# Kernel tuning notes

Hardware: AMD Instinct MI355X
Metric: run time of the kernel (lower is better)

Reference implementation:

```python
import jax, jax.numpy as jnp
import numpy as np

B, K = 2048, 256
ED = RD = HD = 256
AD = ED + RD          # action_dim = 512
IN = ED + HD + RD     # 768
NUM_E, NUM_R = 100000, 500
HUGE = jnp.float32(1e31)  # ops.HUGE_INT


def setup_inputs() -> dict:
    key = jax.random.key(0)
    ks = jax.random.split(key, 12)
    s = 0.05  # keep logits in a sane range
    E = jax.random.normal(ks[0], (B, ED), jnp.float32)
    H = jax.random.normal(ks[1], (B, HD), jnp.float32)
    Q = jax.random.normal(ks[2], (B, RD), jnp.float32)
    W1 = jax.random.normal(ks[3], (AD, IN), jnp.float32) * s
    b1 = jnp.zeros((AD,), jnp.float32)
    W2 = jax.random.normal(ks[4], (AD, AD), jnp.float32) * s
    b2 = jnp.zeros((AD,), jnp.float32)
    emb_r = jax.random.normal(ks[5], (NUM_R, RD), jnp.float32) * s
    emb_e = jax.random.normal(ks[6], (NUM_E, ED), jnp.float32) * s
    # binary action mask (variable-size action spaces, padded); col 0 always valid
    action_mask = (jax.random.uniform(ks[7], (B, K)) > 0.3).astype(jnp.float32)
    action_mask = action_mask.at[:, 0].set(1.0)
    r_space = jax.random.randint(ks[8], (B, K), 0, NUM_R)
    e_space = jax.random.randint(ks[9], (B, K), 0, NUM_E)
    return {"E": E, "H": H, "Q": Q, "W1": W1, "b1": b1, "W2": W2, "b2": b2,
            "emb_r": emb_r, "emb_e": emb_e, "action_mask": action_mask,
            "r_space": r_space, "e_space": e_space}


def reference(E, H, Q, W1, b1, W2, b2, emb_r, emb_e, action_mask, r_space, e_space):
    # state MLP: X = W2Dropout(W2(relu(W1(cat([E, H, Q])))))  (dropout = identity at eval)
    X = jnp.concatenate([E, H, Q], axis=-1)           # [B, IN]
    X = jax.nn.relu(X @ W1.T + b1)                    # [B, AD]
    X2 = X @ W2.T + b2                                # [B, AD]
    # gather action embeddings: A = cat([emb_r[r], emb_e[e]])  [B, K, AD]
    A = jnp.concatenate([emb_r[r_space], emb_e[e_space]], axis=-1)
    # masked softmax over action space
    scores = jnp.einsum('bkd,bd->bk', A, X2) - (1.0 - action_mask) * HUGE
    action_dist = jax.nn.softmax(scores, axis=-1)     # [B, K]
    entropy = -jnp.sum(action_dist * jnp.log(action_dist + 1e-20), axis=-1)  # [B]
    return action_dist, entropy
```

## Files before the change

kernel.cpp:

```cpp
#include <hip/hip_runtime.h>
#include <hip/hip_bf16.h>
#include <hip/hip_fp8.h>
#include <math.h>

#define B_   2048
#define K_   256
#define AD_  512
#define IN_  768
#define NR_  500
#define NRP_ 512
#define NE_  100000

typedef __attribute__((ext_vector_type(8))) short short8;
typedef __attribute__((ext_vector_type(4))) float float4v;

__device__ __forceinline__ unsigned short f2bf(float f) {
    unsigned int u = __float_as_uint(f);
    unsigned int r = u + 0x7FFF + ((u >> 16) & 1);
    return (unsigned short)(r >> 16);
}
__device__ __forceinline__ float bf2f(short s) {
    return __uint_as_float(((unsigned int)(unsigned short)s) << 16);
}
__device__ __forceinline__ unsigned char f2fp8(float f) {
    __hip_fp8_e4m3 t(f);
    return (unsigned char)t.__x;
}
__device__ __forceinline__ float fp8tof(unsigned int byte) {
    __hip_fp8_e4m3 t; t.__x = (__hip_fp8_storage_t)byte; return (float)t;
}
__device__ __forceinline__ float dot4_fp8(unsigned int d, const float* x) {
    return fp8tof(d & 0xffu)         * x[0] + fp8tof((d >> 8) & 0xffu)  * x[1]
         + fp8tof((d >> 16) & 0xffu) * x[2] + fp8tof(d >> 24)           * x[3];
}

#define EE_N4 (NE_ * 256 / 4)
#define X_N4  (B_ * IN_ / 4)
#define W1_N4 (AD_ * IN_ / 4)
#define W2_N4 (AD_ * AD_ / 4)
#define ER_N4 (NR_ * 256 / 4)
#define PREP_TOTAL (EE_N4 + X_N4 + W1_N4 + W2_N4 + ER_N4)
__global__ __launch_bounds__(256) void prep_kernel(
    const float* __restrict__ E, const float* __restrict__ H,
    const float* __restrict__ Q, const float* __restrict__ W1,
    const float* __restrict__ W2, const float* __restrict__ emb_r,
    const float* __restrict__ emb_e,
    ushort* __restrict__ Xb, ushort* __restrict__ W1b,
    ushort* __restrict__ W2b, ushort* __restrict__ emb_rb,
    unsigned char* __restrict__ emb_e8)
{
    int t = blockIdx.x * 256 + threadIdx.x;
    if (t < EE_N4) {
        const float4 v = *(const float4*)&emb_e[(size_t)t * 4];
        uchar4 o;
        o.x = f2fp8(v.x); o.y = f2fp8(v.y); o.z = f2fp8(v.z); o.w = f2fp8(v.w);
        *(uchar4*)&emb_e8[(size_t)t * 4] = o;
        return;
    }
    t -= EE_N4;
    const float* src; ushort* dst; long off;
    if (t < X_N4) {
        const int base = t * 4;
        const int row = base / IN_, col = base % IN_;
        src = (col < 256) ? &E[row * 256 + col]
            : (col < 512) ? &H[row * 256 + col - 256]
                          : &Q[row * 256 + col - 512];
        const float4 v = *(const float4*)src;
        ushort4 o;
        o.x = f2bf(v.x); o.y = f2bf(v.y); o.z = f2bf(v.z); o.w = f2bf(v.w);
        *(ushort4*)&Xb[base] = o;
        return;
    }
    t -= X_N4;
    if (t < W1_N4)                 { src = W1;    dst = W1b;    off = t; }
    else if (t < W1_N4 + W2_N4)    { src = W2;    dst = W2b;    off = t - W1_N4; }
    else if (t < W1_N4 + W2_N4 + ER_N4) { src = emb_r; dst = emb_rb; off = t - W1_N4 - W2_N4; }
    else return;
    const float4 v = *(const float4*)&src[off * 4];
    ushort4 o;
    o.x = f2bf(v.x); o.y = f2bf(v.y); o.z = f2bf(v.z); o.w = f2bf(v.w);
    *(ushort4*)&dst[off * 4] = o;
}

template<int K, bool RELU, bool OUT_BF16, bool BIAS, bool EMIT_RHALF>
__global__ __launch_bounds__(256) void gemm_bf16_kernel(
    const ushort* __restrict__ A, const ushort* __restrict__ Bw,
    const float* __restrict__ bias, ushort* __restrict__ outb,
    float* __restrict__ outf, ushort* __restrict__ rhalf)
{
    constexpr int PITCH = 72;
    __shared__ ushort Asl[2][64 * PITCH];
    __shared__ ushort Bsl[2][64 * PITCH];
    const int tid = threadIdx.x;
    const int lane = tid & 63, w = tid >> 6;
    const int n0 = blockIdx.x * 64, m0 = blockIdx.y * 64;
    const int lrow = tid >> 2, lcg = (tid & 3) * 16;
    const int q = lane >> 4, l16 = lane & 15;

    const ushort* aptr = &A[(size_t)(m0 + lrow) * K + lcg];
    const ushort* bptr = &Bw[(size_t)(n0 + lrow) * K + lcg];

    short8 ra0 = *(const short8*)aptr;
    short8 ra1 = *(const short8*)(aptr + 8);
    short8 rb0 = *(const short8*)bptr;
    short8 rb1 = *(const short8*)(bptr + 8);
    *(short8*)&Asl[0][lrow * PITCH + lcg]     = ra0;
    *(short8*)&Asl[0][lrow * PITCH + lcg + 8] = ra1;
    *(short8*)&Bsl[0][lrow * PITCH + lcg]     = rb0;
    *(short8*)&Bsl[0][lrow * PITCH + lcg + 8] = rb1;

    float4v acc[4] = {};
    int buf = 0;
    __syncthreads();
    for (int k0 = 0; k0 < K; k0 += 64) {
        if (k0 + 64 < K) {
            ra0 = *(const short8*)(aptr + k0 + 64);
            ra1 = *(const short8*)(aptr + k0 + 64 + 8);
            rb0 = *(const short8*)(bptr + k0 + 64);
            rb1 = *(const short8*)(bptr + k0 + 64 + 8);
        }
        #pragma unroll
        for (int kh = 0; kh < 64; kh += 32) {
            const short8 af = *(const short8*)&Asl[buf][(w * 16 + l16) * PITCH + kh + q * 8];
            #pragma unroll
            for (int jn = 0; jn < 4; ++jn) {
                const short8 bfr = *(const short8*)&Bsl[buf][(jn * 16 + l16) * PITCH + kh + q * 8];
                acc[jn] = __builtin_amdgcn_mfma_f32_16x16x32_bf16(af, bfr, acc[jn], 0, 0, 0);
            }
        }
        if (k0 + 64 < K) {
            *(short8*)&Asl[buf ^ 1][lrow * PITCH + lcg]     = ra0;
            *(short8*)&Asl[buf ^ 1][lrow * PITCH + lcg + 8] = ra1;
            *(short8*)&Bsl[buf ^ 1][lrow * PITCH + lcg]     = rb0;
            *(short8*)&Bsl[buf ^ 1][lrow * PITCH + lcg + 8] = rb1;
            __syncthreads();
            buf ^= 1;
        }
    }
    #pragma unroll
    for (int jn = 0; jn < 4; ++jn) {
        const int n = n0 + jn * 16 + l16;
        const float bn = BIAS ? bias[n] : 0.0f;
        #pragma unroll
        for (int r = 0; r < 4; ++r) {
            const int m = m0 + w * 16 + q * 4 + r;
            float c = acc[jn][r] + bn;
            if (RELU) c = fmaxf(c, 0.0f);
            if (OUT_BF16) outb[(size_t)m * AD_ + n] = f2bf(c);
            else if (!EMIT_RHALF || n >= 256) outf[(size_t)m * AD_ + n] = c;
            if (EMIT_RHALF && n < 256) rhalf[(size_t)m * 256 + n] = f2bf(c);
        }
    }
}

__global__ __launch_bounds__(256) void scores_kernel(
    const float* __restrict__ X2, const float* __restrict__ R,
    const unsigned char* __restrict__ emb_e8, const float* __restrict__ mask,
    const int* __restrict__ r_space, const int* __restrict__ e_space,
    float* __restrict__ dist, float* __restrict__ entropy)
{
    const int b = blockIdx.x;
    const int tid = threadIdx.x;
    const int lane = tid & 63, wid = tid >> 6;
    const int l16 = lane & 15, q4 = lane >> 4;

    __shared__ int   s_e[K_];
    __shared__ float s_dot[K_];
    __shared__ float s_red[12];

    const int   e_mine = e_space[b * K_ + tid];
    const int   r_mine = r_space[b * K_ + tid];
    const float mk     = mask[b * K_ + tid];
    s_e[tid] = (mk != 0.0f) ? e_mine : 0;
    const float bias   = R[(size_t)b * NRP_ + r_mine] - (1.0f - mk) * 1e31f;
    float x[16];
    #pragma unroll
    for (int i = 0; i < 4; ++i) {
        const float4 xv = *(const float4*)&X2[(size_t)b * AD_ + 256 + l16 * 16 + i * 4];
        x[i * 4 + 0] = xv.x; x[i * 4 + 1] = xv.y;
        x[i * 4 + 2] = xv.z; x[i * 4 + 3] = xv.w;
    }
    __syncthreads();

    const int kbase = wid * 64;
    #pragma unroll
    for (int it = 0; it < 2; ++it) {
        uint4 wv[8];
        #pragma unroll
        for (int u = 0; u < 8; ++u) {
            const int row = kbase + it * 32 + u * 4 + q4;
            const int e = s_e[row];
            wv[u] = *(const uint4*)&emb_e8[(size_t)e * 256 + l16 * 16];
        }
        float p[8];
        #pragma unroll
        for (int u = 0; u < 8; ++u) {
            p[u] = dot4_fp8(wv[u].x, &x[0]) + dot4_fp8(wv[u].y, &x[4])
                 + dot4_fp8(wv[u].z, &x[8]) + dot4_fp8(wv[u].w, &x[12]);
        }
        #pragma unroll
        for (int off = 8; off >= 1; off >>= 1) {
            #pragma unroll
            for (int u = 0; u < 8; ++u) p[u] += __shfl_down(p[u], off, 16);
        }
        if (l16 == 0) {
            #pragma unroll
            for (int u = 0; u < 8; ++u) s_dot[kbase + it * 32 + u * 4 + q4] = p[u];
        }
    }
    __syncthreads();

    const float v = s_dot[tid] + bias;

    float m = v;
    #pragma unroll
    for (int off = 32; off >= 1; off >>= 1) m = fmaxf(m, __shfl_down(m, off));
    if (lane == 0) s_red[wid] = m;
    __syncthreads();
    if (tid == 0)
        s_red[8] = fmaxf(fmaxf(s_red[0], s_red[1]), fmaxf(s_red[2], s_red[3]));
    __syncthreads();
    const float bmax = s_red[8];

    const float ev = __expf(v - bmax);
    float s = ev;
    float t = ev * (v - bmax);
    #pragma unroll
    for (int off = 32; off >= 1; off >>= 1) {
        s += __shfl_down(s, off);
        t += __shfl_down(t, off);
    }
    if (lane == 0) { s_red[wid] = s; s_red[4 + wid] = t; }
    __syncthreads();
    if (tid == 0) {
        s_red[9]  = s_red[0] + s_red[1] + s_red[2] + s_red[3];
        s_red[10] = s_red[4] + s_red[5] + s_red[6] + s_red[7];
    }
    __syncthreads();
    const float ssum = s_red[9];

    dist[(size_t)b * K_ + tid] = ev / ssum;
    if (tid == 0)
        entropy[b] = logf(ssum) - s_red[10] / ssum;
}

extern "C" void kernel_launch(void* const* d_in, const int* in_sizes, int n_in,
                              void* d_out, int out_size, void* d_ws, size_t ws_size,
                              hipStream_t stream) {
    const float* E     = (const float*)d_in[0];
    const float* H     = (const float*)d_in[1];
    const float* Q     = (const float*)d_in[2];
    const float* W1    = (const float*)d_in[3];
    const float* b1    = (const float*)d_in[4];
    const float* W2    = (const float*)d_in[5];
    const float* b2    = (const float*)d_in[6];
    const float* emb_r = (const float*)d_in[7];
    const float* emb_e = (const float*)d_in[8];
    const float* mask  = (const float*)d_in[9];
    const int* r_space = (const int*)d_in[10];
    const int* e_space = (const int*)d_in[11];

    float* out_dist = (float*)d_out;
    float* out_ent  = out_dist + (size_t)B_ * K_;

    char* ws = (char*)d_ws;
    ushort* Xb     = (ushort*)ws;         ws += (size_t)B_ * IN_ * 2;
    ushort* W1b    = (ushort*)ws;         ws += (size_t)AD_ * IN_ * 2;
    ushort* W2b    = (ushort*)ws;         ws += (size_t)AD_ * AD_ * 2;
    ushort* emb_rb = (ushort*)ws;         ws += (size_t)NRP_ * 256 * 2;
    unsigned char* emb_e8 = (unsigned char*)ws; ws += (size_t)NE_ * 256;
    ushort* H1b    = (ushort*)ws;         ws += (size_t)B_ * AD_ * 2;
    float*  X2     = (float*)ws;          ws += (size_t)B_ * AD_ * 4;
    ushort* X2rb   = (ushort*)ws;         ws += (size_t)B_ * 256 * 2;
    float*  Rt     = (float*)ws;          ws += (size_t)B_ * NRP_ * 4;

    prep_kernel<<<(PREP_TOTAL + 255) / 256, 256, 0, stream>>>(
        E, H, Q, W1, W2, emb_r, emb_e, Xb, W1b, W2b, emb_rb, emb_e8);

    dim3 g(AD_ / 64, B_ / 64);
    gemm_bf16_kernel<IN_, true,  true,  true,  false><<<g, 256, 0, stream>>>(
        Xb, W1b, b1, H1b, nullptr, nullptr);
    gemm_bf16_kernel<AD_, false, false, true,  true ><<<g, 256, 0, stream>>>(
        H1b, W2b, b2, nullptr, X2, X2rb);
    gemm_bf16_kernel<256, false, false, false, false><<<dim3(NRP_ / 64, B_ / 64), 256, 0, stream>>>(
        X2rb, emb_rb, nullptr, nullptr, Rt, nullptr);

    scores_kernel<<<B_, 256, 0, stream>>>(X2, Rt, emb_e8, mask,
                                          r_space, e_space, out_dist, out_ent);
}
```

Baseline: 219.1 us.

## Overlap emb_e fp8 conversion with the three GEMM launches

Moves the 100k×256 emb_e fp32→fp8 conversion out of the prep kernel and splits it into three ranges. Each range is handled by extra blocks (blockIdx.x >= 8) appended to one of the three GEMM launches. The grid widens to 16×32, so conversion blocks run alongside the GEMM blocks and use the bandwidth the small GEMMs leave idle. The conversion uses nontemporal loads with 4x unrolling. The risk is that the conversion blocks compete with the GEMM blocks for CUs and stretch the GEMM critical path.

```diff
diff --git a/kernel.cpp b/kernel.cpp
--- a/kernel.cpp
+++ b/kernel.cpp
@@ -13,6 +13,7 @@
 
 typedef __attribute__((ext_vector_type(8))) short short8;
 typedef __attribute__((ext_vector_type(4))) float float4v;
+typedef __attribute__((ext_vector_type(4))) float f32x4;
 
 __device__ __forceinline__ unsigned short f2bf(float f) {
     unsigned int u = __float_as_uint(f);
@@ -34,30 +35,19 @@
          + fp8tof((d >> 16) & 0xffu) * x[2] + fp8tof(d >> 24)           * x[3];
 }
 
-#define EE_N4 (NE_ * 256 / 4)
 #define X_N4  (B_ * IN_ / 4)
 #define W1_N4 (AD_ * IN_ / 4)
 #define W2_N4 (AD_ * AD_ / 4)
 #define ER_N4 (NR_ * 256 / 4)
-#define PREP_TOTAL (EE_N4 + X_N4 + W1_N4 + W2_N4 + ER_N4)
-__global__ __launch_bounds__(256) void prep_kernel(
+#define PREPS_TOTAL (X_N4 + W1_N4 + W2_N4 + ER_N4)
+__global__ __launch_bounds__(256) void prep_small_kernel(
     const float* __restrict__ E, const float* __restrict__ H,
     const float* __restrict__ Q, const float* __restrict__ W1,
     const float* __restrict__ W2, const float* __restrict__ emb_r,
-    const float* __restrict__ emb_e,
     ushort* __restrict__ Xb, ushort* __restrict__ W1b,
-    ushort* __restrict__ W2b, ushort* __restrict__ emb_rb,
-    unsigned char* __restrict__ emb_e8)
+    ushort* __restrict__ W2b, ushort* __restrict__ emb_rb)
 {
     int t = blockIdx.x * 256 + threadIdx.x;
-    if (t < EE_N4) {
-        const float4 v = *(const float4*)&emb_e[(size_t)t * 4];
-        uchar4 o;
-        o.x = f2fp8(v.x); o.y = f2fp8(v.y); o.z = f2fp8(v.z); o.w = f2fp8(v.w);
-        *(uchar4*)&emb_e8[(size_t)t * 4] = o;
-        return;
-    }
-    t -= EE_N4;
     const float* src; ushort* dst; long off;
     if (t < X_N4) {
         const int base = t * 4;
@@ -82,15 +72,52 @@
     *(ushort4*)&dst[off * 4] = o;
 }
 
+#define EE_N4 (NE_ * 256 / 4)
+__device__ __forceinline__ void conv_range(
+    const float* __restrict__ emb_e, unsigned char* __restrict__ emb_e8,
+    int q0, int q1, int cb)
+{
+    const int stride = 256 * 256;
+    const f32x4* __restrict__ src = (const f32x4*)emb_e;
+    uchar4* __restrict__ dst = (uchar4*)emb_e8;
+    int i = q0 + cb * 256 + (int)threadIdx.x;
+    for (; i + 3 * stride < q1; i += 4 * stride) {
+        f32x4 v0 = __builtin_nontemporal_load(src + i);
+        f32x4 v1 = __builtin_nontemporal_load(src + i + stride);
+        f32x4 v2 = __builtin_nontemporal_load(src + i + 2 * stride);
+        f32x4 v3 = __builtin_nontemporal_load(src + i + 3 * stride);
+        uchar4 o0, o1, o2, o3;
+        o0.x = f2fp8(v0[0]); o0.y = f2fp8(v0[1]); o0.z = f2fp8(v0[2]); o0.w = f2fp8(v0[3]);
+        o1.x = f2fp8(v1[0]); o1.y = f2fp8(v1[1]); o1.z = f2fp8(v1[2]); o1.w = f2fp8(v1[3]);
+        o2.x = f2fp8(v2[0]); o2.y = f2fp8(v2[1]); o2.z = f2fp8(v2[2]); o2.w = f2fp8(v2[3]);
+        o3.x = f2fp8(v3[0]); o3.y = f2fp8(v3[1]); o3.z = f2fp8(v3[2]); o3.w = f2fp8(v3[3]);
+        dst[i] = o0; dst[i + stride] = o1; dst[i + 2 * stride] = o2; dst[i + 3 * stride] = o3;
+    }
+    for (; i < q1; i += stride) {
+        f32x4 v = __builtin_nontemporal_load(src + i);
+        uchar4 o;
+        o.x = f2fp8(v[0]); o.y = f2fp8(v[1]); o.z = f2fp8(v[2]); o.w = f2fp8(v[3]);
+        dst[i] = o;
+    }
+}
+
 template<int K, bool RELU, bool OUT_BF16, bool BIAS, bool EMIT_RHALF>
 __global__ __launch_bounds__(256) void gemm_bf16_kernel(
     const ushort* __restrict__ A, const ushort* __restrict__ Bw,
     const float* __restrict__ bias, ushort* __restrict__ outb,
-    float* __restrict__ outf, ushort* __restrict__ rhalf)
+    float* __restrict__ outf, ushort* __restrict__ rhalf,
+    const float* __restrict__ emb_e, unsigned char* __restrict__ emb_e8,
+    int q0, int q1)
 {
     constexpr int PITCH = 72;
     __shared__ ushort Asl[2][64 * PITCH];
     __shared__ ushort Bsl[2][64 * PITCH];
+
+    if (blockIdx.x >= 8) {
+        conv_range(emb_e, emb_e8, q0, q1, (int)(blockIdx.x - 8) * 32 + (int)blockIdx.y);
+        return;
+    }
+
     const int tid = threadIdx.x;
     const int lane = tid & 63, w = tid >> 6;
     const int n0 = blockIdx.x * 64, m0 = blockIdx.y * 64;
@@ -274,16 +301,19 @@
     ushort* X2rb   = (ushort*)ws;         ws += (size_t)B_ * 256 * 2;
     float*  Rt     = (float*)ws;          ws += (size_t)B_ * NRP_ * 4;
 
-    prep_kernel<<<(PREP_TOTAL + 255) / 256, 256, 0, stream>>>(
-        E, H, Q, W1, W2, emb_r, emb_e, Xb, W1b, W2b, emb_rb, emb_e8);
-
-    dim3 g(AD_ / 64, B_ / 64);
+    const int Q1 = 65536 * 40;
+    const int Q2 = 65536 * 70;
+
+    prep_small_kernel<<<(PREPS_TOTAL + 255) / 256, 256, 0, stream>>>(
+        E, H, Q, W1, W2, emb_r, Xb, W1b, W2b, emb_rb);
+
+    dim3 g(16, 32);
     gemm_bf16_kernel<IN_, true,  true,  true,  false><<<g, 256, 0, stream>>>(
-        Xb, W1b, b1, H1b, nullptr, nullptr);
+        Xb, W1b, b1, H1b, nullptr, nullptr, emb_e, emb_e8, 0, Q1);
     gemm_bf16_kernel<AD_, false, false, true,  true ><<<g, 256, 0, stream>>>(
-        H1b, W2b, b2, nullptr, X2, X2rb);
-    gemm_bf16_kernel<256, false, false, false, false><<<dim3(NRP_ / 64, B_ / 64), 256, 0, stream>>>(
-        X2rb, emb_rb, nullptr, nullptr, Rt, nullptr);
+        H1b, W2b, b2, nullptr, X2, X2rb, emb_e, emb_e8, Q1, Q2);
+    gemm_bf16_kernel<256, false, false, false, false><<<g, 256, 0, stream>>>(
+        X2rb, emb_rb, nullptr, nullptr, Rt, nullptr, emb_e, emb_e8, Q2, EE_N4);
 
     scores_kernel<<<B_, 256, 0, stream>>>(X2, Rt, emb_e8, mask,
                                           r_space, e_space, out_dist, out_ent);
```

After: 211.0 us. 3.7% less time.
